# Kernel tuning notes

Measured on AMD Instinct MI355X. Metric: run time of the kernel, lower is better.

## Reference

```python
import jax, jax.numpy as jnp
import numpy as np

B, T, F = 32, 64, 128          # batch, time_steps, input_dim
H = 8                           # feat_dim (GRU hidden, MHA embed)
NH, HD = 4, 2                   # num_heads, head_dim
HID = 32                        # hidden_dim (out_proj out-features)


def setup_inputs() -> dict:
    key = jax.random.key(0)
    ks = jax.random.split(key, 16)
    s = 0.1
    inp = {
        'x': jax.random.normal(ks[0], (B, T, F), jnp.float32),
        # input_proj: Linear(F, F)
        'Wp': jax.random.normal(ks[1], (F, F), jnp.float32) * s,
        'bp': jax.random.normal(ks[2], (F,), jnp.float32) * s,
        # per-feature GRU weights stacked over F (input size 1 -> squeeze)
        'W_ih': jax.random.normal(ks[3], (F, 3 * H), jnp.float32) * s,
        'b_ih': jax.random.normal(ks[4], (F, 3 * H), jnp.float32) * s,
        'W_hh': jax.random.normal(ks[5], (F, 3 * H, H), jnp.float32) * s,
        'b_hh': jax.random.normal(ks[6], (F, 3 * H), jnp.float32) * s,
        # shared MultiheadAttention (embed=H, heads=NH)
        'in_w': jax.random.normal(ks[7], (3 * H, H), jnp.float32) * s,
        'in_b': jax.random.normal(ks[8], (3 * H,), jnp.float32) * s,
        'ow': jax.random.normal(ks[9], (H, H), jnp.float32) * s,
        'ob': jax.random.normal(ks[10], (H,), jnp.float32) * s,
        # out_proj: Linear(F*H, HID)
        'Wout': jax.random.normal(ks[11], (HID, F * H), jnp.float32) * s,
        'bout': jax.random.normal(ks[12], (HID,), jnp.float32) * s,
    }
    return inp


def _forward(x, Wp, bp, W_ih, b_ih, W_hh, b_hh, in_w, in_b, ow, ob, Wout, bout):
    xp = x @ Wp.T + bp                               # [B,T,F] input_proj

    # ---- batched per-feature GRU (vectorized over B and F, scan over T) ----
    def step(h, x_t):                                # h [B,F,H], x_t [B,F]
        gx = x_t[..., None] * W_ih + b_ih            # [B,F,3H]
        gh = jnp.einsum('bfh,fgh->bfg', h, W_hh) + b_hh
        r = jax.nn.sigmoid(gx[..., :H] + gh[..., :H])
        z = jax.nn.sigmoid(gx[..., H:2 * H] + gh[..., H:2 * H])
        n = jnp.tanh(gx[..., 2 * H:] + r * gh[..., 2 * H:])
        h_new = (1.0 - z) * n + z * h
        return h_new, h_new

    h0 = jnp.zeros((x.shape[0], F, H), x.dtype)
    _, hs = jax.lax.scan(step, h0, jnp.moveaxis(xp, 1, 0))   # [T,B,F,H]
    out = jnp.moveaxis(hs, 0, 1)                              # [B,T,F,H]

    # ---- shared MHA over time, batched across (B, F) ----
    seq = out.transpose(0, 2, 1, 3)                           # [B,F,T,H]
    qkv = seq @ in_w.T + in_b                                 # [B,F,T,3H]
    q, k, v = jnp.split(qkv, 3, axis=-1)
    def heads(t):  # [B,F,T,H] -> [B,F,T,NH,HD]
        return t.reshape(t.shape[:-1] + (NH, HD))
    q, k, v = heads(q), heads(k), heads(v)
    scale = 1.0 / np.sqrt(HD)
    scores = jnp.einsum('bfqnd,bfknd->bfnqk', q, k) * scale   # [B,F,NH,T,T]
    w = jax.nn.softmax(scores, axis=-1)
    ctx = jnp.einsum('bfnqk,bfknd->bfqnd', w, v)
    ctx = ctx.reshape(ctx.shape[:2] + (ctx.shape[2], H))      # [B,F,T,H]
    attn_out = ctx @ ow.T + ob                                # [B,F,T,H]
    attention = attn_out.transpose(0, 2, 1, 3)                # [B,T,F,H]

    # ---- flatten GRU outputs and project ----
    y = out.reshape(out.shape[0], out.shape[1], F * H) @ Wout.T + bout  # [B,T,HID]
    return y, attention


def reference(x, Wp, bp, W_ih, b_ih, W_hh, b_hh, in_w, in_b, ow, ob, Wout, bout):
    return _forward(x, Wp, bp, W_ih, b_ih, W_hh, b_hh, in_w, in_b, ow, ob, Wout, bout)
```

## Files before the change

### kernel.cpp

```cpp
#include <hip/hip_runtime.h>


namespace {
constexpr int Bb = 32, Tt = 64, Ff = 128, Hh = 8, HIDh = 32;
constexpr int G3H = 24;
constexpr float L2E = 1.44269504088896340736f;
constexpr int XPS = 0;
constexpr int UB  = 132;
constexpr int UBS = 772;
constexpr int KV  = 132 + 2 * 772;
constexpr int KK0 = KV, KK1 = KV + 272, VV0 = KV + 544, VV1 = KV + 816;
constexpr int SM_SIZE = KV + 1088;
}

__device__ __forceinline__ float rcp_(float x) {
#if __has_builtin(__builtin_amdgcn_rcpf)
  return __builtin_amdgcn_rcpf(x);
#else
  return 1.0f / x;
#endif
}
__device__ __forceinline__ float exp2_(float x) {
#if __has_builtin(__builtin_amdgcn_exp2f)
  return __builtin_amdgcn_exp2f(x);
#else
  return exp2f(x);
#endif
}

#define MHA_STEP(K0C, K1C, V0C, V1C)                         \
  {                                                          \
    _Pragma("unroll") for (int i = 0; i < 4; ++i) {          \
      float s = fmaf(q0[i], K0C, q1[i] * K1C);               \
      float p = exp2_(s);                                    \
      ps[i] += p;                                            \
      c0[i] = fmaf(p, V0C, c0[i]);                           \
      c1[i] = fmaf(p, V1C, c1[i]);                           \
    }                                                        \
  }

__global__ __launch_bounds__(64) void k_fused(
    const float* __restrict__ x, const float* __restrict__ Wp, const float* __restrict__ bp,
    const float* __restrict__ W_ih, const float* __restrict__ b_ih,
    const float* __restrict__ W_hh, const float* __restrict__ b_hh,
    const float* __restrict__ in_w, const float* __restrict__ in_b,
    const float* __restrict__ ow, const float* __restrict__ ob,
    float* __restrict__ outp, float* __restrict__ attn) {
  __shared__ float smem[SM_SIZE];
  const int t = threadIdx.x;
  const int blk = blockIdx.x;
  const int b = blk >> 6;
  const int f0 = (blk & 63) * 2;

  {
    const float4* xr = (const float4*)(x + (b * Tt + t) * Ff);
    const float4* wA = (const float4*)(Wp + f0 * Ff);
    const float4* wB = (const float4*)(Wp + (f0 + 1) * Ff);
    float a0 = bp[f0], a1 = bp[f0 + 1];
#pragma unroll 8
    for (int k = 0; k < Ff / 4; ++k) {
      float4 xv = xr[k], va = wA[k], vb = wB[k];
      a0 = fmaf(xv.x, va.x, a0); a0 = fmaf(xv.y, va.y, a0);
      a0 = fmaf(xv.z, va.z, a0); a0 = fmaf(xv.w, va.w, a0);
      a1 = fmaf(xv.x, vb.x, a1); a1 = fmaf(xv.y, vb.y, a1);
      a1 = fmaf(xv.z, vb.z, a1); a1 = fmaf(xv.w, vb.w, a1);
    }
    smem[XPS + t] = a0;
    smem[XPS + 65 + t] = a1;
  }
  asm volatile("s_waitcnt lgkmcnt(0)" ::: "memory");

  if (t < 16) {
    __builtin_amdgcn_s_setprio(1);
    const int g = t >> 3, j = t & 7;
    const int f = f0 + g;
    const float* wb = W_hh + (f * G3H + j) * Hh;
    const float nL = -L2E, S2 = 2.0f * L2E;
    float w0s[8], w1s[8], w2s[8];
#pragma unroll
    for (int h = 0; h < 8; ++h) {
      w0s[h] = wb[h] * nL;
      w1s[h] = wb[64 + h] * nL;
      w2s[h] = wb[128 + h] * S2;
    }
    const float wi0s = W_ih[f * G3H + j] * nL;
    const float wi1s = W_ih[f * G3H + 8 + j] * nL;
    const float wi2s = W_ih[f * G3H + 16 + j] * S2;
    const float bias_r = (b_ih[f * G3H + j] + b_hh[f * G3H + j]) * nL;
    const float bias_z = (b_ih[f * G3H + 8 + j] + b_hh[f * G3H + 8 + j]) * nL;
    const float bi2s = b_ih[f * G3H + 16 + j] * S2;
    const float bh2s = b_hh[f * G3H + 16 + j] * S2;
    float hall[8];
#pragma unroll
    for (int h = 0; h < 8; ++h) hall[h] = 0.f;
    float h_own = 0.f;
    const int base = t & 56;
    float* hdst = &smem[UB + g * UBS + j];
    const float* xps = &smem[XPS + g * 65];
    for (int tt = 0; tt < Tt; ++tt) {
      float xt = xps[tt];
      float a0 = bias_r, a1 = bias_z, a2 = bh2s;
#pragma unroll
      for (int h = 0; h < 8; ++h) {
        a0 = fmaf(hall[h], w0s[h], a0);
        a1 = fmaf(hall[h], w1s[h], a1);
        a2 = fmaf(hall[h], w2s[h], a2);
      }
      float r = rcp_(1.0f + exp2_(fmaf(xt, wi0s, a0)));
      float z = rcp_(1.0f + exp2_(fmaf(xt, wi1s, a1)));
      float narg = fmaf(r, a2, fmaf(xt, wi2s, bi2s));
      float n = fmaf(-2.0f, rcp_(exp2_(narg) + 1.0f), 1.0f);
      float hn = fmaf(z, h_own - n, n);
      hdst[tt * 12] = hn;
      h_own = hn;
#pragma unroll
      for (int h = 0; h < 8; ++h) hall[h] = __shfl(hn, base + h, 64);
    }
    __builtin_amdgcn_s_setprio(0);
  }
  asm volatile("s_waitcnt lgkmcnt(0)" ::: "memory");

  {
    float4* og = (float4*)(outp + (b * Ff + f0) * Tt * Hh);
#pragma unroll
    for (int i = 0; i < 4; ++i) {
      int v = i * 64 + t;
      int fl = v >> 7, rem = v & 127;
      int tt = rem >> 1, j0 = (rem & 1) * 4;
      og[v] = *(const float4*)&smem[UB + fl * UBS + tt * 12 + j0];
    }
  }
  asm volatile("s_waitcnt lgkmcnt(0)" ::: "memory");

  constexpr float SCL = 0.70710678118654752f * L2E;
#pragma unroll
  for (int fl = 0; fl < 2; ++fl) {
    float* ub = &smem[UB + fl * UBS];
    float sq[8];
    *(float4*)&sq[0] = *(const float4*)&ub[t * 12];
    *(float4*)&sq[4] = *(const float4*)&ub[t * 12 + 4];
    float qv[8], ka[8], va[8];
#pragma unroll
    for (int jj = 0; jj < 8; ++jj) {
      float aq = in_b[jj], ak = in_b[8 + jj], av = in_b[16 + jj];
#pragma unroll
      for (int h = 0; h < 8; ++h) {
        aq = fmaf(sq[h], in_w[jj * 8 + h], aq);
        ak = fmaf(sq[h], in_w[(8 + jj) * 8 + h], ak);
        av = fmaf(sq[h], in_w[(16 + jj) * 8 + h], av);
      }
      qv[jj] = aq * SCL; ka[jj] = ak; va[jj] = av;
    }
    *(float4*)&ub[t * 12] = make_float4(qv[0], qv[1], qv[2], qv[3]);
    *(float4*)&ub[t * 12 + 4] = make_float4(qv[4], qv[5], qv[6], qv[7]);
#pragma unroll
    for (int n = 0; n < 4; ++n) {
      smem[KK0 + n * 68 + t] = ka[2 * n];
      smem[KK1 + n * 68 + t] = ka[2 * n + 1];
      smem[VV0 + n * 68 + t] = va[2 * n];
      smem[VV1 + n * 68 + t] = va[2 * n + 1];
    }
    asm volatile("s_waitcnt lgkmcnt(0)" ::: "memory");

    {
      const int n = t >> 4, qq = t & 15;
      float q0[4], q1[4];
#pragma unroll
      for (int i = 0; i < 4; ++i) {
        float2 qp = *(const float2*)&ub[(qq + 16 * i) * 12 + 2 * n];
        q0[i] = qp.x; q1[i] = qp.y;
      }
      float ps[4], c0[4], c1[4];
#pragma unroll
      for (int i = 0; i < 4; ++i) { ps[i] = 0.f; c0[i] = 0.f; c1[i] = 0.f; }
#pragma unroll 2
      for (int kt4 = 0; kt4 < Tt; kt4 += 4) {
        float4 k0 = *(const float4*)&smem[KK0 + n * 68 + kt4];
        float4 k1 = *(const float4*)&smem[KK1 + n * 68 + kt4];
        float4 v0 = *(const float4*)&smem[VV0 + n * 68 + kt4];
        float4 v1 = *(const float4*)&smem[VV1 + n * 68 + kt4];
        MHA_STEP(k0.x, k1.x, v0.x, v1.x)
        MHA_STEP(k0.y, k1.y, v0.y, v1.y)
        MHA_STEP(k0.z, k1.z, v0.z, v1.z)
        MHA_STEP(k0.w, k1.w, v0.w, v1.w)
      }
#pragma unroll
      for (int i = 0; i < 4; ++i) {
        float inv = rcp_(ps[i]);
        *(float2*)&ub[(qq + 16 * i) * 12 + 2 * n] =
            make_float2(c0[i] * inv, c1[i] * inv);
      }
    }
    asm volatile("s_waitcnt lgkmcnt(0)" ::: "memory");

    {
      float cx[8];
      *(float4*)&cx[0] = *(const float4*)&ub[t * 12];
      *(float4*)&cx[4] = *(const float4*)&ub[t * 12 + 4];
      float o8[8];
#pragma unroll
      for (int jj = 0; jj < 8; ++jj) {
        float a = ob[jj];
#pragma unroll
        for (int h = 0; h < 8; ++h) a = fmaf(cx[h], ow[jj * 8 + h], a);
        o8[jj] = a;
      }
      *(float4*)&ub[t * 12] = make_float4(o8[0], o8[1], o8[2], o8[3]);
      *(float4*)&ub[t * 12 + 4] = make_float4(o8[4], o8[5], o8[6], o8[7]);
    }
    asm volatile("s_waitcnt lgkmcnt(0)" ::: "memory");
  }

  {
#pragma unroll
    for (int i = 0; i < 4; ++i) {
      int v = i * 64 + t;
      int tt = v >> 2, c = v & 3;
      int fl = c >> 1, h0 = (c & 1) * 4;
      float4 val = *(const float4*)&smem[UB + fl * UBS + tt * 12 + h0];
      *(float4*)(attn + ((b * Tt + tt) * Ff + f0 + fl) * Hh + h0) = val;
    }
  }
}

__global__ __launch_bounds__(128) void k_outproj(
    const float* __restrict__ outp, const float* __restrict__ Wout,
    const float* __restrict__ bout, float* __restrict__ y) {
  constexpr int TT = 8;
  int blk = blockIdx.x;
  int b = blk >> 3;
  int t0 = (blk & 7) * TT;
  int tid = threadIdx.x;
  int oq = tid >> 4;
  int fc = tid & 15;
  float acc[TT][4];
#pragma unroll
  for (int tt = 0; tt < TT; ++tt)
#pragma unroll
    for (int od = 0; od < 4; ++od) acc[tt][od] = 0.f;
#pragma unroll
  for (int ff = 0; ff < 8; ++ff) {
    int f = fc * 8 + ff;
    const float4* rb = (const float4*)(outp + ((b * Ff + f) * Tt + t0) * Hh);
    float4 rv[16];
#pragma unroll
    for (int i = 0; i < 16; ++i) rv[i] = rb[i];
#pragma unroll
    for (int od = 0; od < 4; ++od) {
      int o = oq * 4 + od;
      const float4* wbp = (const float4*)(Wout + o * (Ff * Hh) + f * Hh);
      float4 wa = wbp[0], wc = wbp[1];
#pragma unroll
      for (int tt = 0; tt < TT; ++tt) {
        float4 ra = rv[tt * 2], rc = rv[tt * 2 + 1];
        float s = acc[tt][od];
        s = fmaf(ra.x, wa.x, s); s = fmaf(ra.y, wa.y, s);
        s = fmaf(ra.z, wa.z, s); s = fmaf(ra.w, wa.w, s);
        s = fmaf(rc.x, wc.x, s); s = fmaf(rc.y, wc.y, s);
        s = fmaf(rc.z, wc.z, s); s = fmaf(rc.w, wc.w, s);
        acc[tt][od] = s;
      }
    }
  }
#pragma unroll
  for (int tt = 0; tt < TT; ++tt)
#pragma unroll
    for (int od = 0; od < 4; ++od) {
      float v = acc[tt][od];
      v += __shfl_xor(v, 1, 16);
      v += __shfl_xor(v, 2, 16);
      v += __shfl_xor(v, 4, 16);
      v += __shfl_xor(v, 8, 16);
      acc[tt][od] = v;
    }
#pragma unroll
  for (int tt = 0; tt < TT; ++tt) {
    if (fc == tt) {
#pragma unroll
      for (int od = 0; od < 4; ++od) {
        int o = oq * 4 + od;
        y[(b * Tt + t0 + tt) * HIDh + o] = acc[tt][od] + bout[o];
      }
    }
  }
}

extern "C" void kernel_launch(void* const* d_in, const int* in_sizes, int n_in,
                              void* d_out, int out_size, void* d_ws, size_t ws_size,
                              hipStream_t stream) {
  (void)in_sizes; (void)n_in; (void)out_size; (void)ws_size;
  const float* x    = (const float*)d_in[0];
  const float* Wp   = (const float*)d_in[1];
  const float* bp   = (const float*)d_in[2];
  const float* W_ih = (const float*)d_in[3];
  const float* b_ih = (const float*)d_in[4];
  const float* W_hh = (const float*)d_in[5];
  const float* b_hh = (const float*)d_in[6];
  const float* in_w = (const float*)d_in[7];
  const float* in_b = (const float*)d_in[8];
  const float* ow   = (const float*)d_in[9];
  const float* ob   = (const float*)d_in[10];
  const float* Wout = (const float*)d_in[11];
  const float* bout = (const float*)d_in[12];

  float* y    = (float*)d_out;
  float* attn = (float*)d_out + Bb * Tt * HIDh;
  float* outp = (float*)d_ws;

  hipLaunchKernelGGL(k_fused, dim3(Bb * (Ff / 2)), dim3(64), 0, stream,
                     x, Wp, bp, W_ih, b_ih, W_hh, b_hh, in_w, in_b, ow, ob, outp, attn);
  hipLaunchKernelGGL(k_outproj, dim3(Bb * (Tt / 8)), dim3(128), 0, stream,
                     outp, Wout, bout, y);
}
```

Measured before the change: 64.97 us.

## Process four features per block with one wave per feature for projection and MHA

The fused kernel now uses 256-thread blocks covering four features instead of 64-thread blocks covering two. Each wave computes one feature's input projection and runs that feature's attention in parallel, while 32 lanes of the first wave run the four GRU recurrences. The GRU output is stored time-contiguous per hidden unit, and the q/context staging moves to a separate region, with __syncthreads between phases. This aims to spread the projection and attention work across more waves and halve the block count, at the cost of block-wide barriers, more LDS per block, and three waves idling during the serial GRU loop.

```diff
diff --git a/kernel.cpp b/kernel.cpp
--- a/kernel.cpp
+++ b/kernel.cpp
@@ -5,12 +5,11 @@
 constexpr int Bb = 32, Tt = 64, Ff = 128, Hh = 8, HIDh = 32;
 constexpr int G3H = 24;
 constexpr float L2E = 1.44269504088896340736f;
-constexpr int XPS = 0;
-constexpr int UB  = 132;
-constexpr int UBS = 772;
-constexpr int KV  = 132 + 2 * 772;
-constexpr int KK0 = KV, KK1 = KV + 272, VV0 = KV + 544, VV1 = KV + 816;
-constexpr int SM_SIZE = KV + 1088;
+constexpr int XPS  = 0;
+constexpr int HOUT = 260;
+constexpr int OCT  = 2340;
+constexpr int KV   = 4900;
+constexpr int SM_SIZE = KV + 4 * 1088;
 }
 
 __device__ __forceinline__ float rcp_(float x) {
@@ -39,7 +38,7 @@
     }                                                        \
   }
 
-__global__ __launch_bounds__(64) void k_fused(
+__global__ __launch_bounds__(256, 4) void k_fused(
     const float* __restrict__ x, const float* __restrict__ Wp, const float* __restrict__ bp,
     const float* __restrict__ W_ih, const float* __restrict__ b_ih,
     const float* __restrict__ W_hh, const float* __restrict__ b_hh,
@@ -47,30 +46,29 @@
     const float* __restrict__ ow, const float* __restrict__ ob,
     float* __restrict__ outp, float* __restrict__ attn) {
   __shared__ float smem[SM_SIZE];
-  const int t = threadIdx.x;
+  const int tid = threadIdx.x;
+  const int t = tid & 63;
+  const int w = tid >> 6;
   const int blk = blockIdx.x;
-  const int b = blk >> 6;
-  const int f0 = (blk & 63) * 2;
+  const int b = blk >> 5;
+  const int f0 = (blk & 31) * 4;
 
   {
+    const int f = f0 + w;
     const float4* xr = (const float4*)(x + (b * Tt + t) * Ff);
-    const float4* wA = (const float4*)(Wp + f0 * Ff);
-    const float4* wB = (const float4*)(Wp + (f0 + 1) * Ff);
-    float a0 = bp[f0], a1 = bp[f0 + 1];
+    const float4* wr = (const float4*)(Wp + f * Ff);
+    float acc = bp[f];
 #pragma unroll 8
     for (int k = 0; k < Ff / 4; ++k) {
-      float4 xv = xr[k], va = wA[k], vb = wB[k];
-      a0 = fmaf(xv.x, va.x, a0); a0 = fmaf(xv.y, va.y, a0);
-      a0 = fmaf(xv.z, va.z, a0); a0 = fmaf(xv.w, va.w, a0);
-      a1 = fmaf(xv.x, vb.x, a1); a1 = fmaf(xv.y, vb.y, a1);
-      a1 = fmaf(xv.z, vb.z, a1); a1 = fmaf(xv.w, vb.w, a1);
-    }
-    smem[XPS + t] = a0;
-    smem[XPS + 65 + t] = a1;
-  }
-  asm volatile("s_waitcnt lgkmcnt(0)" ::: "memory");
-
-  if (t < 16) {
+      float4 xv = xr[k], wv = wr[k];
+      acc = fmaf(xv.x, wv.x, acc); acc = fmaf(xv.y, wv.y, acc);
+      acc = fmaf(xv.z, wv.z, acc); acc = fmaf(xv.w, wv.w, acc);
+    }
+    smem[XPS + w * 65 + t] = acc;
+  }
+  __syncthreads();
+
+  if (tid < 32) {
     __builtin_amdgcn_s_setprio(1);
     const int g = t >> 3, j = t & 7;
     const int f = f0 + g;
@@ -95,7 +93,7 @@
     for (int h = 0; h < 8; ++h) hall[h] = 0.f;
     float h_own = 0.f;
     const int base = t & 56;
-    float* hdst = &smem[UB + g * UBS + j];
+    float* hdst = &smem[HOUT + g * 520 + j * 65];
     const float* xps = &smem[XPS + g * 65];
     for (int tt = 0; tt < Tt; ++tt) {
       float xt = xps[tt];
@@ -111,34 +109,39 @@
       float narg = fmaf(r, a2, fmaf(xt, wi2s, bi2s));
       float n = fmaf(-2.0f, rcp_(exp2_(narg) + 1.0f), 1.0f);
       float hn = fmaf(z, h_own - n, n);
-      hdst[tt * 12] = hn;
+      hdst[tt] = hn;
       h_own = hn;
 #pragma unroll
       for (int h = 0; h < 8; ++h) hall[h] = __shfl(hn, base + h, 64);
     }
     __builtin_amdgcn_s_setprio(0);
   }
-  asm volatile("s_waitcnt lgkmcnt(0)" ::: "memory");
+  __syncthreads();
 
   {
-    float4* og = (float4*)(outp + (b * Ff + f0) * Tt * Hh);
-#pragma unroll
-    for (int i = 0; i < 4; ++i) {
-      int v = i * 64 + t;
+    float4* og = (float4*)(outp + (size_t)(b * Ff + f0) * Tt * Hh);
+#pragma unroll
+    for (int i = 0; i < 2; ++i) {
+      int v = i * 256 + tid;
       int fl = v >> 7, rem = v & 127;
       int tt = rem >> 1, j0 = (rem & 1) * 4;
-      og[v] = *(const float4*)&smem[UB + fl * UBS + tt * 12 + j0];
-    }
-  }
-  asm volatile("s_waitcnt lgkmcnt(0)" ::: "memory");
-
-  constexpr float SCL = 0.70710678118654752f * L2E;
-#pragma unroll
-  for (int fl = 0; fl < 2; ++fl) {
-    float* ub = &smem[UB + fl * UBS];
+      const float* hp = &smem[HOUT + fl * 520 + j0 * 65 + tt];
+      og[v] = make_float4(hp[0], hp[65], hp[130], hp[195]);
+    }
+  }
+
+  {
+    constexpr float SCL = 0.70710678118654752f * L2E;
+    const float* hsrc = &smem[HOUT + w * 520];
+    float* oc = &smem[OCT + w * 640];
+    float* kk0 = &smem[KV + w * 1088];
+    float* kk1 = kk0 + 272;
+    float* vv0 = kk0 + 544;
+    float* vv1 = kk0 + 816;
+
     float sq[8];
-    *(float4*)&sq[0] = *(const float4*)&ub[t * 12];
-    *(float4*)&sq[4] = *(const float4*)&ub[t * 12 + 4];
+#pragma unroll
+    for (int h = 0; h < 8; ++h) sq[h] = hsrc[h * 65 + t];
     float qv[8], ka[8], va[8];
 #pragma unroll
     for (int jj = 0; jj < 8; ++jj) {
@@ -151,52 +154,51 @@
       }
       qv[jj] = aq * SCL; ka[jj] = ak; va[jj] = av;
     }
-    *(float4*)&ub[t * 12] = make_float4(qv[0], qv[1], qv[2], qv[3]);
-    *(float4*)&ub[t * 12 + 4] = make_float4(qv[4], qv[5], qv[6], qv[7]);
 #pragma unroll
     for (int n = 0; n < 4; ++n) {
-      smem[KK0 + n * 68 + t] = ka[2 * n];
-      smem[KK1 + n * 68 + t] = ka[2 * n + 1];
-      smem[VV0 + n * 68 + t] = va[2 * n];
-      smem[VV1 + n * 68 + t] = va[2 * n + 1];
+      *(float2*)&oc[t * 10 + 2 * n] = make_float2(qv[2 * n], qv[2 * n + 1]);
+      kk0[n * 68 + t] = ka[2 * n];
+      kk1[n * 68 + t] = ka[2 * n + 1];
+      vv0[n * 68 + t] = va[2 * n];
+      vv1[n * 68 + t] = va[2 * n + 1];
     }
     asm volatile("s_waitcnt lgkmcnt(0)" ::: "memory");
 
+    const int n = t >> 4, qq = t & 15;
+    float q0[4], q1[4];
+#pragma unroll
+    for (int i = 0; i < 4; ++i) {
+      float2 qp = *(const float2*)&oc[(qq + 16 * i) * 10 + 2 * n];
+      q0[i] = qp.x; q1[i] = qp.y;
+    }
+    float ps[4], c0[4], c1[4];
+#pragma unroll
+    for (int i = 0; i < 4; ++i) { ps[i] = 0.f; c0[i] = 0.f; c1[i] = 0.f; }
+#pragma unroll 2
+    for (int kt4 = 0; kt4 < Tt; kt4 += 4) {
+      float4 k0 = *(const float4*)&kk0[n * 68 + kt4];
+      float4 k1 = *(const float4*)&kk1[n * 68 + kt4];
+      float4 v0 = *(const float4*)&vv0[n * 68 + kt4];
+      float4 v1 = *(const float4*)&vv1[n * 68 + kt4];
+      MHA_STEP(k0.x, k1.x, v0.x, v1.x)
+      MHA_STEP(k0.y, k1.y, v0.y, v1.y)
+      MHA_STEP(k0.z, k1.z, v0.z, v1.z)
+      MHA_STEP(k0.w, k1.w, v0.w, v1.w)
+    }
+#pragma unroll
+    for (int i = 0; i < 4; ++i) {
+      float inv = rcp_(ps[i]);
+      *(float2*)&oc[(qq + 16 * i) * 10 + 2 * n] =
+          make_float2(c0[i] * inv, c1[i] * inv);
+    }
+    asm volatile("s_waitcnt lgkmcnt(0)" ::: "memory");
+
     {
-      const int n = t >> 4, qq = t & 15;
-      float q0[4], q1[4];
-#pragma unroll
-      for (int i = 0; i < 4; ++i) {
-        float2 qp = *(const float2*)&ub[(qq + 16 * i) * 12 + 2 * n];
-        q0[i] = qp.x; q1[i] = qp.y;
-      }
-      float ps[4], c0[4], c1[4];
-#pragma unroll
-      for (int i = 0; i < 4; ++i) { ps[i] = 0.f; c0[i] = 0.f; c1[i] = 0.f; }
-#pragma unroll 2
-      for (int kt4 = 0; kt4 < Tt; kt4 += 4) {
-        float4 k0 = *(const float4*)&smem[KK0 + n * 68 + kt4];
-        float4 k1 = *(const float4*)&smem[KK1 + n * 68 + kt4];
-        float4 v0 = *(const float4*)&smem[VV0 + n * 68 + kt4];
-        float4 v1 = *(const float4*)&smem[VV1 + n * 68 + kt4];
-        MHA_STEP(k0.x, k1.x, v0.x, v1.x)
-        MHA_STEP(k0.y, k1.y, v0.y, v1.y)
-        MHA_STEP(k0.z, k1.z, v0.z, v1.z)
-        MHA_STEP(k0.w, k1.w, v0.w, v1.w)
-      }
-#pragma unroll
-      for (int i = 0; i < 4; ++i) {
-        float inv = rcp_(ps[i]);
-        *(float2*)&ub[(qq + 16 * i) * 12 + 2 * n] =
-            make_float2(c0[i] * inv, c1[i] * inv);
-      }
-    }
-    asm volatile("s_waitcnt lgkmcnt(0)" ::: "memory");
-
-    {
-      float cx[8];
-      *(float4*)&cx[0] = *(const float4*)&ub[t * 12];
-      *(float4*)&cx[4] = *(const float4*)&ub[t * 12 + 4];
+      float2 cp0 = *(const float2*)&oc[t * 10 + 0];
+      float2 cp1 = *(const float2*)&oc[t * 10 + 2];
+      float2 cp2 = *(const float2*)&oc[t * 10 + 4];
+      float2 cp3 = *(const float2*)&oc[t * 10 + 6];
+      float cx[8] = {cp0.x, cp0.y, cp1.x, cp1.y, cp2.x, cp2.y, cp3.x, cp3.y};
       float o8[8];
 #pragma unroll
       for (int jj = 0; jj < 8; ++jj) {
@@ -205,20 +207,23 @@
         for (int h = 0; h < 8; ++h) a = fmaf(cx[h], ow[jj * 8 + h], a);
         o8[jj] = a;
       }
-      *(float4*)&ub[t * 12] = make_float4(o8[0], o8[1], o8[2], o8[3]);
-      *(float4*)&ub[t * 12 + 4] = make_float4(o8[4], o8[5], o8[6], o8[7]);
-    }
-    asm volatile("s_waitcnt lgkmcnt(0)" ::: "memory");
-  }
+      *(float2*)&oc[t * 10 + 0] = make_float2(o8[0], o8[1]);
+      *(float2*)&oc[t * 10 + 2] = make_float2(o8[2], o8[3]);
+      *(float2*)&oc[t * 10 + 4] = make_float2(o8[4], o8[5]);
+      *(float2*)&oc[t * 10 + 6] = make_float2(o8[6], o8[7]);
+    }
+  }
+  __syncthreads();
 
   {
 #pragma unroll
-    for (int i = 0; i < 4; ++i) {
-      int v = i * 64 + t;
-      int tt = v >> 2, c = v & 3;
+    for (int i = 0; i < 2; ++i) {
+      int v = i * 256 + tid;
+      int tt = v >> 3, c = v & 7;
       int fl = c >> 1, h0 = (c & 1) * 4;
-      float4 val = *(const float4*)&smem[UB + fl * UBS + tt * 12 + h0];
-      *(float4*)(attn + ((b * Tt + tt) * Ff + f0 + fl) * Hh + h0) = val;
+      const float* sp = &smem[OCT + fl * 640 + tt * 10 + h0];
+      float4 val = make_float4(sp[0], sp[1], sp[2], sp[3]);
+      *(float4*)(attn + (((size_t)b * Tt + tt) * Ff + f0 + fl) * Hh + h0) = val;
     }
   }
 }
@@ -307,7 +312,7 @@
   float* attn = (float*)d_out + Bb * Tt * HIDh;
   float* outp = (float*)d_ws;
 
-  hipLaunchKernelGGL(k_fused, dim3(Bb * (Ff / 2)), dim3(64), 0, stream,
+  hipLaunchKernelGGL(k_fused, dim3(Bb * (Ff / 4)), dim3(256), 0, stream,
                      x, Wp, bp, W_ih, b_ih, W_hh, b_hh, in_w, in_b, ow, ob, outp, attn);
   hipLaunchKernelGGL(k_outproj, dim3(Bb * (Tt / 8)), dim3(128), 0, stream,
                      outp, Wout, bout, y);
```

Result: faster. 61.93 us (-4.7%).
